# Kernel optimization log

Measured on AMD Instinct MI355X. Metric: run time of the kernel, lower is better.

Reference implementation:

```python
import jax, jax.numpy as jnp
import numpy as np

THRESH = 0.5   # global `thresh` used by ActFun
LENS = 0.5     # global `lens` (surrogate width)
DECAY = 0.25   # LIFNode init_decay
INV_STD = 1.0 / float(np.sqrt(1.0 + 1e-5))  # BN eval: running_mean=0, running_var=1
HEADS = 8
WINDOW = 8

@jax.custom_vjp
def act_fun(x):
    return (x > THRESH).astype(x.dtype)

def _act_fwd(x):
    return act_fun(x), x

def _act_bwd(x, g):
    temp = (jnp.abs(x - THRESH) < LENS).astype(g.dtype) / (2.0 * LENS)
    return (g * temp,)

act_fun.defvjp(_act_fwd, _act_bwd)

def lif(x):
    # x: [T, ...]; mem = x[0]; mem_t = mem_{t-1}*decay*(1-spike_{t-1}.detach()) + x_t
    spike0 = act_fun(x[0])
    def step(carry, xi):
        mem_prev, spike_prev = carry
        mem = mem_prev * DECAY * (1.0 - jax.lax.stop_gradient(spike_prev)) + xi
        spike = act_fun(mem)
        return (mem, spike), spike
    _, spikes = jax.lax.scan(step, (x[0], spike0), x[1:])
    return jnp.concatenate([spike0[None], spikes], axis=0)

def bn_eval(x, gamma, beta):
    # BatchNorm2d eval over channel D (last dim of [T,B,L,D]) with default running stats
    return x * (INV_STD * gamma) + beta

def linear(x, w, b):
    # torch nn.Linear: y = x @ w.T + b, w: [out, in]
    return jnp.einsum('tbld,ed->tble', x, w) + b


def setup_inputs() -> dict:
    key = jax.random.key(0)
    ks = jax.random.split(key, 12)
    T, B, L, D = 4, 4, 1024, 512
    s = 0.02
    inp = {
        'x': jax.random.normal(ks[0], (T, B, L, D), dtype=jnp.float32),
        'pos_bias': jax.random.uniform(ks[1], (L, L), dtype=jnp.float32),
        'q_w': jax.random.normal(ks[2], (D, D), dtype=jnp.float32) * s,
        'q_b': jnp.zeros((D,), jnp.float32),
        'q_g': jnp.ones((D,), jnp.float32),
        'q_beta': jnp.zeros((D,), jnp.float32),
        'k_w': jax.random.normal(ks[3], (D, D), dtype=jnp.float32) * s,
        'k_b': jnp.zeros((D,), jnp.float32),
        'k_g': jnp.ones((D,), jnp.float32),
        'k_beta': jnp.zeros((D,), jnp.float32),
        'v_w': jax.random.normal(ks[4], (D, D), dtype=jnp.float32) * s,
        'v_b': jnp.zeros((D,), jnp.float32),
        'v_g': jnp.ones((D,), jnp.float32),
        'v_beta': jnp.zeros((D,), jnp.float32),
        'last_w': jax.random.normal(ks[5], (D, D), dtype=jnp.float32) * s,
        'last_b': jnp.zeros((D,), jnp.float32),
        'last_g': jnp.ones((D,), jnp.float32),
        'last_beta': jnp.zeros((D,), jnp.float32),
    }
    return inp


def reference(x, pos_bias, q_w, q_b, q_g, q_beta, k_w, k_b, k_g, k_beta,
              v_w, v_b, v_g, v_beta, last_w, last_b, last_g, last_beta):
    T, B, L, D = x.shape
    H = HEADS
    Dh = D // H
    # local causal band: keep pos_bias[i,j] only where 0 <= i-j < WINDOW
    i = jnp.arange(L)[:, None]
    j = jnp.arange(L)[None, :]
    band = ((i - j) >= 0) & ((i - j) < WINDOW)
    pb = jnp.where(band, pos_bias[:L, :L], 0.0)  # [L, L]

    xs = lif(x)  # first_lif
    q = lif(bn_eval(linear(xs, q_w, q_b), q_g, q_beta))
    k = lif(bn_eval(linear(xs, k_w, k_b), k_g, k_beta))
    v = lif(bn_eval(linear(xs, v_w, v_b), v_g, v_beta))

    # [T,B,L,D] -> [T,B,L,H,Dh] -> [B,H,L,T,Dh] -> [B,H,L,T*Dh]
    qh = q.reshape(T, B, L, H, Dh).transpose(1, 3, 2, 0, 4).reshape(B, H, L, T * Dh)
    kv = (k * v).reshape(T, B, L, H, Dh).transpose(1, 3, 2, 0, 4).reshape(B, H, L, T * Dh)

    attn = jnp.einsum('ij,bhjd->bhid', pb, kv)  # local-window positional mixing
    out = qh * attn
    out = out.reshape(B, H, L, T, Dh).transpose(3, 0, 2, 1, 4).reshape(T, B, L, D)
    out = lif(out)  # attn_lif
    out = bn_eval(linear(out, last_w, last_b), last_g, last_beta)
    return out
```

## Files before the change

kernel.cpp:

```cpp
#include <hip/hip_runtime.h>
#include <stdint.h>


#define T_ 4
#define B_ 4
#define L_ 1024
#define D_ 512
#define BI_ (B_*L_)
#define STRIDE4 (B_*L_*D_/4)
#define INV_STD 0.9999950000374997f
#define EPS_FLAG 1e-3f
#define LIST_CAP 5000000u

typedef unsigned int   u32;
typedef unsigned char  u8;
typedef int i32x4 __attribute__((ext_vector_type(4)));

static __device__ __forceinline__ float spike_of(float m) {
  return m > 0.5f ? 1.0f : 0.0f;
}

__global__ __launch_bounds__(256) void k_wsplit(const float* __restrict__ qw,
    const float* __restrict__ kw, const float* __restrict__ vw,
    const float* __restrict__ lw, u8* __restrict__ Wq,
    float* __restrict__ scl, u32* __restrict__ cnt) {
  if (blockIdx.x == 0 && threadIdx.x == 0) *cnt = 0;
  int gid = blockIdx.x * 4 + (threadIdx.x >> 6);
  int mat = gid >> 9, e = gid & 511;
  int lane = threadIdx.x & 63;
  const float* W = mat == 0 ? qw : mat == 1 ? kw : mat == 2 ? vw : lw;
  const float4* w4 = (const float4*)(W + (size_t)e * 512 + lane * 8);
  float4 wa = w4[0], wb = w4[1];
  float w[8] = {wa.x, wa.y, wa.z, wa.w, wb.x, wb.y, wb.z, wb.w};
  float am = 0.f;
#pragma unroll
  for (int j = 0; j < 8; ++j) am = fmaxf(am, fabsf(w[j]));
#pragma unroll
  for (int off = 1; off < 64; off <<= 1)
    am = fmaxf(am, __shfl_xor(am, off, 64));
  float s1 = am > 0.f ? am * (1.0f / 127.0f) : 1.0f;
  float s2 = s1 * (1.0f / 254.0f);
  float inv1 = 1.0f / s1, inv2 = 1.0f / s2;
  u32 p1lo = 0, p1hi = 0, p2lo = 0, p2hi = 0;
#pragma unroll
  for (int j = 0; j < 8; ++j) {
    float q1 = rintf(w[j] * inv1);
    q1 = fminf(127.f, fmaxf(-127.f, q1));
    float r = w[j] - s1 * q1;
    float q2 = rintf(r * inv2);
    q2 = fminf(127.f, fmaxf(-127.f, q2));
    u32 b1 = (u32)(u8)(signed char)(int)q1;
    u32 b2 = (u32)(u8)(signed char)(int)q2;
    if (j < 4) { p1lo |= b1 << (j * 8); p2lo |= b2 << (j * 8); }
    else       { p1hi |= b1 << ((j - 4) * 8); p2hi |= b2 << ((j - 4) * 8); }
  }
  u8* base = Wq + (size_t)mat * 524288 + (size_t)(e >> 6) * 65536 +
             (size_t)(lane >> 1) * 1024 + (size_t)(e & 63) * 16 + (lane & 1) * 8;
  *(uint2*)base             = make_uint2(p1lo, p1hi);
  *(uint2*)(base + 32768)   = make_uint2(p2lo, p2hi);
  if (lane == 0) {
    scl[mat * 1024 + e] = s1;
    scl[mat * 1024 + 512 + e] = s2;
  }
}

__global__ __launch_bounds__(256) void k_lif_first(const float* __restrict__ x,
                                                   u8* __restrict__ xsb) {
  int idx = blockIdx.x * 256 + threadIdx.x;
  if (idx >= STRIDE4) return;
  const int bi = idx >> 7, d4 = idx & 127;
  const float4* x4 = (const float4*)x;
  uchar4* o4 = (uchar4*)xsb;
  float m[4], s[4];
  float4 v = x4[idx];
  m[0] = v.x; m[1] = v.y; m[2] = v.z; m[3] = v.w;
#pragma unroll
  for (int c = 0; c < 4; ++c) s[c] = spike_of(m[c]);
  o4[(bi * 4 + 0) * 128 + d4] =
      make_uchar4((u8)s[0], (u8)s[1], (u8)s[2], (u8)s[3]);
#pragma unroll
  for (int t = 1; t < T_; ++t) {
    v = x4[idx + t * STRIDE4];
    float xv[4] = {v.x, v.y, v.z, v.w};
#pragma unroll
    for (int c = 0; c < 4; ++c) {
      m[c] = m[c] * 0.25f * (1.0f - s[c]) + xv[c];
      s[c] = spike_of(m[c]);
    }
    o4[(bi * 4 + t) * 128 + d4] =
        make_uchar4((u8)s[0], (u8)s[1], (u8)s[2], (u8)s[3]);
  }
}

__device__ __forceinline__ void gemm_flat(const u8* __restrict__ Ab,
    const u8* __restrict__ Wc, int rowbase, int la, int lg,
    i32x4 (&acc)[4][4][2]) {
  const u8* ap = Ab + (size_t)(rowbase + la) * 512 + lg * 16;
  const u8* bp = Wc + lg * 1024 + la * 16;

#pragma unroll
  for (int s = 0; s < 4; ++s)
#pragma unroll
    for (int cf = 0; cf < 4; ++cf)
#pragma unroll
      for (int pl = 0; pl < 2; ++pl) acc[s][cf][pl] = (i32x4){0, 0, 0, 0};

  uint4 Abuf[2][4], Bbuf[2][8];
#pragma unroll
  for (int s = 0; s < 4; ++s)
    Abuf[0][s] = *(const uint4*)(ap + s * 8192);
#pragma unroll
  for (int cf = 0; cf < 4; ++cf)
#pragma unroll
    for (int pl = 0; pl < 2; ++pl)
      Bbuf[0][cf * 2 + pl] = *(const uint4*)(bp + pl * 32768 + cf * 256);

#pragma unroll
  for (int ks = 0; ks < 8; ++ks) {
    const int cur = ks & 1, nxt = cur ^ 1;
    if (ks < 7) {
#pragma unroll
      for (int s = 0; s < 4; ++s)
        Abuf[nxt][s] = *(const uint4*)(ap + s * 8192 + (ks + 1) * 64);
#pragma unroll
      for (int cf = 0; cf < 4; ++cf)
#pragma unroll
        for (int pl = 0; pl < 2; ++pl)
          Bbuf[nxt][cf * 2 + pl] =
              *(const uint4*)(bp + (ks + 1) * 4096 + pl * 32768 + cf * 256);
    }
#pragma unroll
    for (int cf = 0; cf < 4; ++cf)
#pragma unroll
      for (int pl = 0; pl < 2; ++pl)
#pragma unroll
        for (int s = 0; s < 4; ++s)
          acc[s][cf][pl] = __builtin_amdgcn_mfma_i32_16x16x64_i8(
              __builtin_bit_cast(i32x4, Abuf[cur][s]),
              __builtin_bit_cast(i32x4, Bbuf[cur][cf * 2 + pl]),
              acc[s][cf][pl], 0, 0, 0);
  }
}

__global__ __launch_bounds__(256) void k_gemm_qkv(const u8* __restrict__ Ab,
    const u8* __restrict__ Wq, const float* __restrict__ scl,
    const float* __restrict__ qb2, const float* __restrict__ qg,
    const float* __restrict__ qbe,
    const float* __restrict__ kb2, const float* __restrict__ kg,
    const float* __restrict__ kbe,
    const float* __restrict__ vb2, const float* __restrict__ vg,
    const float* __restrict__ vbe,
    u8* __restrict__ qs, u8* __restrict__ ks_, u8* __restrict__ vs,
    u32* __restrict__ list, u32* __restrict__ cnt) {
  const int tid = threadIdx.x;
  const int lane = tid & 63, wid = tid >> 6;
  const int la = lane & 15, lg = lane >> 4;
  const int colblk = blockIdx.x;
  const int tz = blockIdx.z;
  const int rowbase = (blockIdx.y * 4 + wid) * 64;
  const u8* Wc = Wq + (size_t)tz * 524288 + (size_t)colblk * 65536;
  const float* Bb = tz == 0 ? qb2 : tz == 1 ? kb2 : vb2;
  const float* Gg = tz == 0 ? qg  : tz == 1 ? kg  : vg;
  const float* Be = tz == 0 ? qbe : tz == 1 ? kbe : vbe;
  u8* S           = tz == 0 ? qs  : tz == 1 ? ks_ : vs;

  i32x4 acc[4][4][2];
  gemm_flat(Ab, Wc, rowbase, la, lg, acc);

#pragma unroll
  for (int cf = 0; cf < 4; ++cf) {
    int e = colblk * 64 + cf * 16 + la;
    float s1 = scl[tz * 1024 + e];
    float s2 = scl[tz * 1024 + 512 + e];
    float cs = INV_STD * Gg[e];
    float cb = Bb[e], ct = Be[e];
#pragma unroll
    for (int s = 0; s < 4; ++s) {
      int r0 = rowbase + s * 16 + lg * 4;
      int bi = r0 >> 2;
      float m = 0.f, sp = 0.f;
      int fl = 0;
#pragma unroll
      for (int p = 0; p < 4; ++p) {
        float raw = s1 * (float)acc[s][cf][0][p] + s2 * (float)acc[s][cf][1][p];
        float pre = (raw + cb) * cs + ct;
        if (p == 0) m = pre;
        else m = m * 0.25f * (1.0f - sp) + pre;
        sp = spike_of(m);
        if (fabsf(m - 0.5f) < EPS_FLAG) fl = 1;
        S[(size_t)(r0 + p) * 512 + e] = (u8)sp;
      }
      if (fl) {
        u32 pos = atomicAdd(cnt, 1u);
        if (pos < LIST_CAP)
          list[pos] = ((u32)tz << 21) | (u32)(bi * 512 + e);
      }
    }
  }
}

__global__ __launch_bounds__(256) void k_gemm_out(const u8* __restrict__ Ab,
    const u8* __restrict__ Wq, const float* __restrict__ scl,
    const float* __restrict__ bias, const float* __restrict__ gamma,
    const float* __restrict__ beta, float* __restrict__ Y) {
  const int tid = threadIdx.x;
  const int lane = tid & 63, wid = tid >> 6;
  const int la = lane & 15, lg = lane >> 4;
  const int colblk = blockIdx.x;
  const int rowbase = (blockIdx.y * 4 + wid) * 64;
  const u8* Wc = Wq + 3u * 524288 + (size_t)colblk * 65536;

  i32x4 acc[4][4][2];
  gemm_flat(Ab, Wc, rowbase, la, lg, acc);

#pragma unroll
  for (int cf = 0; cf < 4; ++cf) {
    int e = colblk * 64 + cf * 16 + la;
    float s1 = scl[3 * 1024 + e];
    float s2 = scl[3 * 1024 + 512 + e];
    float cs = INV_STD * gamma[e];
    float cb = bias[e], ct = beta[e];
#pragma unroll
    for (int s = 0; s < 4; ++s) {
      int r0 = rowbase + s * 16 + lg * 4;
      int bi = r0 >> 2;
#pragma unroll
      for (int p = 0; p < 4; ++p) {
        float raw = s1 * (float)acc[s][cf][0][p] + s2 * (float)acc[s][cf][1][p];
        Y[((size_t)p * BI_ + bi) * 512 + e] = (raw + cb) * cs + ct;
      }
    }
  }
}

__device__ __forceinline__ void consume32_u8(const float4 (&wb)[8],
                                             const uint4 (&ab)[2], float& c) {
#pragma unroll
  for (int u = 0; u < 8; ++u) {
    float4 w = wb[u];
    uint4 t = ab[u >> 2];
    u32 word = (u & 3) == 0 ? t.x : (u & 3) == 1 ? t.y
             : (u & 3) == 2 ? t.z : t.w;
    c += (word & 0xFFu)       ? w.x : 0.0f;
    c += (word & 0xFF00u)     ? w.y : 0.0f;
    c += (word & 0xFF0000u)   ? w.z : 0.0f;
    c += (word >> 24)         ? w.w : 0.0f;
  }
}

__global__ __launch_bounds__(128) void k_fixup_c(const u8* __restrict__ xsb,
    u8* __restrict__ qs, u8* __restrict__ ks, u8* __restrict__ vs,
    const float* __restrict__ qw, const float* __restrict__ qb2,
    const float* __restrict__ qg, const float* __restrict__ qbe,
    const float* __restrict__ kw, const float* __restrict__ kb2,
    const float* __restrict__ kg, const float* __restrict__ kbe,
    const float* __restrict__ vw, const float* __restrict__ vb2,
    const float* __restrict__ vg, const float* __restrict__ vbe,
    const u32* __restrict__ list, const u32* __restrict__ cnt) {
  u32 n = *cnt;
  if (n > LIST_CAP) n = LIST_CAP;
  u32 tot = n * 4;
  for (u32 ii = blockIdx.x * 128 + threadIdx.x; ii < tot;
       ii += gridDim.x * 128) {
    u32 i = ii >> 2;
    int t = (int)(ii & 3);
    u32 e = list[i];
    int tz = (int)(e >> 21);
    int col = (int)(e & 0x1FFFFFu);
    int bi = col >> 9, d = col & 511;
    const float* W  = tz == 0 ? qw  : tz == 1 ? kw  : vw;
    const float* Bb = tz == 0 ? qb2 : tz == 1 ? kb2 : vb2;
    const float* Gg = tz == 0 ? qg  : tz == 1 ? kg  : vg;
    const float* Be = tz == 0 ? qbe : tz == 1 ? kbe : vbe;
    u8* S           = tz == 0 ? qs  : tz == 1 ? ks  : vs;
    const float4* w4 = (const float4*)(W + (size_t)d * 512);
    const uint4*  R  = (const uint4*)(xsb + ((size_t)bi * 4 + t) * 512);

    float4 wA[8], wB[8];
    uint4 aA[2], aB[2];
#pragma unroll
    for (int u = 0; u < 8; ++u) wA[u] = w4[u];
#pragma unroll
    for (int u = 0; u < 2; ++u) aA[u] = R[u];
    float c = 0.f;
#pragma unroll
    for (int ch = 0; ch < 16; ++ch) {
      if ((ch & 1) == 0) {
        if (ch + 1 < 16) {
          int wb0 = (ch + 1) * 8, ab0 = (ch + 1) * 2;
#pragma unroll
          for (int u = 0; u < 8; ++u) wB[u] = w4[wb0 + u];
#pragma unroll
          for (int u = 0; u < 2; ++u) aB[u] = R[ab0 + u];
        }
        consume32_u8(wA, aA, c);
      } else {
        if (ch + 1 < 16) {
          int wb0 = (ch + 1) * 8, ab0 = (ch + 1) * 2;
#pragma unroll
          for (int u = 0; u < 8; ++u) wA[u] = w4[wb0 + u];
#pragma unroll
          for (int u = 0; u < 2; ++u) aA[u] = R[ab0 + u];
        }
        consume32_u8(wB, aB, c);
      }
    }
    int lane = threadIdx.x & 63;
    int qb = lane & ~3;
    float cq[4];
    cq[0] = __shfl(c, qb + 0, 64);
    cq[1] = __shfl(c, qb + 1, 64);
    cq[2] = __shfl(c, qb + 2, 64);
    cq[3] = __shfl(c, qb + 3, 64);
    float cs = INV_STD * Gg[d];
    float cb = Bb[d], ct = Be[d];
    float m = 0.f, s = 0.f;
    u8 myb = 0;
#pragma unroll
    for (int t2 = 0; t2 < 4; ++t2) {
      float pre = (cq[t2] + cb) * cs + ct;
      if (t2 == 0) m = pre;
      else m = m * 0.25f * (1.0f - s) + pre;
      s = spike_of(m);
      if (t2 == t) myb = (u8)s;
    }
    S[((size_t)bi * 4 + t) * 512 + d] = myb;
  }
}

__global__ __launch_bounds__(256) void k_attn(const u8* __restrict__ qs,
    const u8* __restrict__ ks, const u8* __restrict__ vs,
    const float* __restrict__ pos_bias, u8* __restrict__ sout) {
  int idx = blockIdx.x * 256 + threadIdx.x;
  if (idx >= STRIDE4) return;
  const int d4 = idx & 127;
  const int bi = idx >> 7;
  const int i = bi & (L_ - 1);
  const int wmax = i < 7 ? i : 7;

  float pbv[8];
  const float* pbrow = pos_bias + (size_t)i * L_ + i;
  for (int w = 0; w <= wmax; ++w) pbv[w] = pbrow[-w];

  const uchar4* k4 = (const uchar4*)ks;
  const uchar4* v4 = (const uchar4*)vs;
  const uchar4* q4 = (const uchar4*)qs;
  float pre[T_][4];

#pragma unroll
  for (int t = 0; t < T_; ++t) {
    float sum[4] = {0.f, 0.f, 0.f, 0.f};
    for (int w = wmax; w >= 0; --w) {
      int rj = ((bi - w) * 4 + t) * 128 + d4;
      uchar4 ku = k4[rj];
      uchar4 vu = v4[rj];
      sum[0] += (ku.x && vu.x) ? pbv[w] : 0.0f;
      sum[1] += (ku.y && vu.y) ? pbv[w] : 0.0f;
      sum[2] += (ku.z && vu.z) ? pbv[w] : 0.0f;
      sum[3] += (ku.w && vu.w) ? pbv[w] : 0.0f;
    }
    uchar4 qu = q4[(bi * 4 + t) * 128 + d4];
    pre[t][0] = qu.x ? sum[0] : 0.0f;
    pre[t][1] = qu.y ? sum[1] : 0.0f;
    pre[t][2] = qu.z ? sum[2] : 0.0f;
    pre[t][3] = qu.w ? sum[3] : 0.0f;
  }

  uchar4* s4 = (uchar4*)sout;
  float m[4], s[4];
#pragma unroll
  for (int c = 0; c < 4; ++c) { m[c] = pre[0][c]; s[c] = spike_of(m[c]); }
  s4[(bi * 4 + 0) * 128 + d4] =
      make_uchar4((u8)s[0], (u8)s[1], (u8)s[2], (u8)s[3]);
#pragma unroll
  for (int t = 1; t < T_; ++t) {
#pragma unroll
    for (int c = 0; c < 4; ++c) {
      m[c] = m[c] * 0.25f * (1.0f - s[c]) + pre[t][c];
      s[c] = spike_of(m[c]);
    }
    s4[(bi * 4 + t) * 128 + d4] =
        make_uchar4((u8)s[0], (u8)s[1], (u8)s[2], (u8)s[3]);
  }
}

extern "C" void kernel_launch(void* const* d_in, const int* in_sizes, int n_in,
                              void* d_out, int out_size, void* d_ws, size_t ws_size,
                              hipStream_t stream) {
  (void)in_sizes; (void)n_in; (void)out_size; (void)ws_size;
  const float* x        = (const float*)d_in[0];
  const float* pos_bias = (const float*)d_in[1];
  const float* q_w    = (const float*)d_in[2];
  const float* q_b    = (const float*)d_in[3];
  const float* q_g    = (const float*)d_in[4];
  const float* q_beta = (const float*)d_in[5];
  const float* k_w    = (const float*)d_in[6];
  const float* k_b    = (const float*)d_in[7];
  const float* k_g    = (const float*)d_in[8];
  const float* k_beta = (const float*)d_in[9];
  const float* v_w    = (const float*)d_in[10];
  const float* v_b    = (const float*)d_in[11];
  const float* v_g    = (const float*)d_in[12];
  const float* v_beta = (const float*)d_in[13];
  const float* last_w    = (const float*)d_in[14];
  const float* last_b    = (const float*)d_in[15];
  const float* last_g    = (const float*)d_in[16];
  const float* last_beta = (const float*)d_in[17];
  float* out = (float*)d_out;

  char* ws = (char*)d_ws;
  u8*    xsb  = (u8*)(ws + 0);
  u8*    qs   = (u8*)(ws + 8388608);
  u8*    ks   = (u8*)(ws + 16777216);
  u8*    vs   = (u8*)(ws + 25165824);
  u8*    sA   = (u8*)(ws + 33554432);
  u8*    Wq   = (u8*)(ws + 41943040);
  float* scl  = (float*)(ws + 46137344);
  u32*   list = (u32*)(ws + 50331648);
  u32*   cnt  = (u32*)(ws + 73400320);

  k_wsplit<<<512, 256, 0, stream>>>(q_w, k_w, v_w, last_w, Wq, scl, cnt);
  k_lif_first<<<2048, 256, 0, stream>>>(x, xsb);

  dim3 gq(8, 64, 3);
  k_gemm_qkv<<<gq, 256, 0, stream>>>(xsb, Wq, scl,
      q_b, q_g, q_beta, k_b, k_g, k_beta, v_b, v_g, v_beta,
      qs, ks, vs, list, cnt);

  k_fixup_c<<<2048, 128, 0, stream>>>(xsb, qs, ks, vs,
      q_w, q_b, q_g, q_beta, k_w, k_b, k_g, k_beta, v_w, v_b, v_g, v_beta,
      list, cnt);

  k_attn<<<2048, 256, 0, stream>>>(qs, ks, vs, pos_bias, sA);

  dim3 gg(8, 64);
  k_gemm_out<<<gg, 256, 0, stream>>>(sA, Wq, scl,
                                     last_b, last_g, last_beta, out);
}
```

Before: 346.2 us.

## Stage weight tile in LDS and coalesce spike stores via shared buffer

Both int8 GEMM kernels now copy their 64 KB weight column-block into LDS with global_load_lds before computing, and read B fragments from LDS instead of global memory. The A-operand double buffering is dropped in favour of direct per-step loads. The QKV kernel stages its spike outputs in a 16 KB shared tile and writes them back as coalesced 16-byte rows, and its grid order changes so blocks sharing a weight tile run close together. The cost is 80 KB of LDS per block, which limits occupancy, plus an up-front barrier-bound load phase.

```diff
diff --git a/kernel.cpp b/kernel.cpp
--- a/kernel.cpp
+++ b/kernel.cpp
@@ -18,6 +18,12 @@
 
 static __device__ __forceinline__ float spike_of(float m) {
   return m > 0.5f ? 1.0f : 0.0f;
+}
+
+__device__ __forceinline__ void gll16(const void* g, void* l) {
+  __builtin_amdgcn_global_load_lds(
+      (const __attribute__((address_space(1))) u32*)g,
+      (__attribute__((address_space(3))) u32*)l, 16, 0, 0);
 }
 
 __global__ __launch_bounds__(256) void k_wsplit(const float* __restrict__ qw,
@@ -92,43 +98,32 @@
   }
 }
 
-__device__ __forceinline__ void gemm_flat(const u8* __restrict__ Ab,
-    const u8* __restrict__ Wc, int rowbase, int la, int lg,
+__device__ __forceinline__ void gemm_wres(const u8* __restrict__ Ab,
+    const u8* __restrict__ smW, int rowbase, int la, int lg,
     i32x4 (&acc)[4][4][2]) {
+#pragma unroll
+  for (int s = 0; s < 4; ++s)
+#pragma unroll
+    for (int cf = 0; cf < 4; ++cf)
+#pragma unroll
+      for (int pl = 0; pl < 2; ++pl) acc[s][cf][pl] = (i32x4){0, 0, 0, 0};
+
   const u8* ap = Ab + (size_t)(rowbase + la) * 512 + lg * 16;
-  const u8* bp = Wc + lg * 1024 + la * 16;
-
-#pragma unroll
-  for (int s = 0; s < 4; ++s)
+  const u8* bp = smW + lg * 1024 + la * 16;
+
+#pragma unroll
+  for (int ks = 0; ks < 8; ++ks) {
+    uint4 Af[4];
+#pragma unroll
+    for (int s = 0; s < 4; ++s)
+      Af[s] = *(const uint4*)(ap + s * 8192 + ks * 64);
+    uint4 Bf[8];
 #pragma unroll
     for (int cf = 0; cf < 4; ++cf)
 #pragma unroll
-      for (int pl = 0; pl < 2; ++pl) acc[s][cf][pl] = (i32x4){0, 0, 0, 0};
-
-  uint4 Abuf[2][4], Bbuf[2][8];
-#pragma unroll
-  for (int s = 0; s < 4; ++s)
-    Abuf[0][s] = *(const uint4*)(ap + s * 8192);
-#pragma unroll
-  for (int cf = 0; cf < 4; ++cf)
-#pragma unroll
-    for (int pl = 0; pl < 2; ++pl)
-      Bbuf[0][cf * 2 + pl] = *(const uint4*)(bp + pl * 32768 + cf * 256);
-
-#pragma unroll
-  for (int ks = 0; ks < 8; ++ks) {
-    const int cur = ks & 1, nxt = cur ^ 1;
-    if (ks < 7) {
-#pragma unroll
-      for (int s = 0; s < 4; ++s)
-        Abuf[nxt][s] = *(const uint4*)(ap + s * 8192 + (ks + 1) * 64);
-#pragma unroll
-      for (int cf = 0; cf < 4; ++cf)
-#pragma unroll
-        for (int pl = 0; pl < 2; ++pl)
-          Bbuf[nxt][cf * 2 + pl] =
-              *(const uint4*)(bp + (ks + 1) * 4096 + pl * 32768 + cf * 256);
-    }
+      for (int pl = 0; pl < 2; ++pl)
+        Bf[cf * 2 + pl] =
+            *(const uint4*)(bp + pl * 32768 + ks * 4096 + cf * 256);
 #pragma unroll
     for (int cf = 0; cf < 4; ++cf)
 #pragma unroll
@@ -136,8 +131,8 @@
 #pragma unroll
         for (int s = 0; s < 4; ++s)
           acc[s][cf][pl] = __builtin_amdgcn_mfma_i32_16x16x64_i8(
-              __builtin_bit_cast(i32x4, Abuf[cur][s]),
-              __builtin_bit_cast(i32x4, Bbuf[cur][cf * 2 + pl]),
+              __builtin_bit_cast(i32x4, Af[s]),
+              __builtin_bit_cast(i32x4, Bf[cf * 2 + pl]),
               acc[s][cf][pl], 0, 0, 0);
   }
 }
@@ -152,20 +147,28 @@
     const float* __restrict__ vbe,
     u8* __restrict__ qs, u8* __restrict__ ks_, u8* __restrict__ vs,
     u32* __restrict__ list, u32* __restrict__ cnt) {
+  __shared__ __align__(16) u8 smW[65536];
+  __shared__ __align__(16) u8 smS[16384];
   const int tid = threadIdx.x;
   const int lane = tid & 63, wid = tid >> 6;
   const int la = lane & 15, lg = lane >> 4;
   const int colblk = blockIdx.x;
-  const int tz = blockIdx.z;
-  const int rowbase = (blockIdx.y * 4 + wid) * 64;
+  const int tz = blockIdx.y;
+  const int row0 = blockIdx.z * 256;
+  const int rowbase = row0 + wid * 64;
   const u8* Wc = Wq + (size_t)tz * 524288 + (size_t)colblk * 65536;
   const float* Bb = tz == 0 ? qb2 : tz == 1 ? kb2 : vb2;
   const float* Gg = tz == 0 ? qg  : tz == 1 ? kg  : vg;
   const float* Be = tz == 0 ? qbe : tz == 1 ? kbe : vbe;
   u8* S           = tz == 0 ? qs  : tz == 1 ? ks_ : vs;
 
+#pragma unroll
+  for (int u = 0; u < 16; ++u)
+    gll16(Wc + u * 4096 + tid * 16, smW + u * 4096 + tid * 16);
+  __syncthreads();
+
   i32x4 acc[4][4][2];
-  gemm_flat(Ab, Wc, rowbase, la, lg, acc);
+  gemm_wres(Ab, smW, rowbase, la, lg, acc);
 
 #pragma unroll
   for (int cf = 0; cf < 4; ++cf) {
@@ -176,8 +179,8 @@
     float cb = Bb[e], ct = Be[e];
 #pragma unroll
     for (int s = 0; s < 4; ++s) {
-      int r0 = rowbase + s * 16 + lg * 4;
-      int bi = r0 >> 2;
+      int rl = wid * 64 + s * 16 + lg * 4;
+      int bi = (row0 + rl) >> 2;
       float m = 0.f, sp = 0.f;
       int fl = 0;
 #pragma unroll
@@ -188,7 +191,7 @@
         else m = m * 0.25f * (1.0f - sp) + pre;
         sp = spike_of(m);
         if (fabsf(m - 0.5f) < EPS_FLAG) fl = 1;
-        S[(size_t)(r0 + p) * 512 + e] = (u8)sp;
+        smS[(rl + p) * 64 + cf * 16 + la] = (u8)sp;
       }
       if (fl) {
         u32 pos = atomicAdd(cnt, 1u);
@@ -197,21 +200,36 @@
       }
     }
   }
+  __syncthreads();
+#pragma unroll
+  for (int ps = 0; ps < 4; ++ps) {
+    int rr = ps * 64 + (tid >> 2);
+    int c16 = (tid & 3) * 16;
+    uint4 vv = *(const uint4*)(smS + rr * 64 + c16);
+    *(uint4*)(S + (size_t)(row0 + rr) * 512 + colblk * 64 + c16) = vv;
+  }
 }
 
 __global__ __launch_bounds__(256) void k_gemm_out(const u8* __restrict__ Ab,
     const u8* __restrict__ Wq, const float* __restrict__ scl,
     const float* __restrict__ bias, const float* __restrict__ gamma,
     const float* __restrict__ beta, float* __restrict__ Y) {
+  __shared__ __align__(16) u8 smW[65536];
   const int tid = threadIdx.x;
   const int lane = tid & 63, wid = tid >> 6;
   const int la = lane & 15, lg = lane >> 4;
   const int colblk = blockIdx.x;
-  const int rowbase = (blockIdx.y * 4 + wid) * 64;
+  const int row0 = blockIdx.y * 256;
+  const int rowbase = row0 + wid * 64;
   const u8* Wc = Wq + 3u * 524288 + (size_t)colblk * 65536;
 
+#pragma unroll
+  for (int u = 0; u < 16; ++u)
+    gll16(Wc + u * 4096 + tid * 16, smW + u * 4096 + tid * 16);
+  __syncthreads();
+
   i32x4 acc[4][4][2];
-  gemm_flat(Ab, Wc, rowbase, la, lg, acc);
+  gemm_wres(Ab, smW, rowbase, la, lg, acc);
 
 #pragma unroll
   for (int cf = 0; cf < 4; ++cf) {
@@ -422,7 +440,7 @@
   k_wsplit<<<512, 256, 0, stream>>>(q_w, k_w, v_w, last_w, Wq, scl, cnt);
   k_lif_first<<<2048, 256, 0, stream>>>(x, xsb);
 
-  dim3 gq(8, 64, 3);
+  dim3 gq(8, 3, 64);
   k_gemm_qkv<<<gq, 256, 0, stream>>>(xsb, Wq, scl,
       q_b, q_g, q_beta, k_b, k_g, k_beta, v_b, v_g, v_beta,
       qs, ks, vs, list, cnt);
```

New measurement: 323.9 us. -6.4%, faster.

## Stage spike rows in LDS and pack q/k/v spikes across time into u32

Applied to the files above, without the earlier changes.

The int8 GEMMs now load a 32-row activation tile into shared memory with global_load_lds and an XOR swizzle. Each block then computes all three q/k/v projections, or the full output width, for that tile. Weights are stored row-major and streamed per wave with register double buffering. The q/k/v spike outputs are packed with all four timesteps in one u32 per (position, channel), so attention loads each neighbour once for all timesteps and the GEMM epilogue does one 32-bit store. The cost is lower grid parallelism (512 blocks), heavier per-block work, and weight reads that are no longer staged in the tiled layout.

```diff
diff --git a/kernel.cpp b/kernel.cpp
--- a/kernel.cpp
+++ b/kernel.cpp
@@ -18,6 +18,12 @@
 
 static __device__ __forceinline__ float spike_of(float m) {
   return m > 0.5f ? 1.0f : 0.0f;
+}
+
+__device__ __forceinline__ void gll16(const void* g, void* l) {
+  __builtin_amdgcn_global_load_lds(
+      (const __attribute__((address_space(1))) u32*)g,
+      (__attribute__((address_space(3))) u32*)l, 16, 0, 0);
 }
 
 __global__ __launch_bounds__(256) void k_wsplit(const float* __restrict__ qw,
@@ -54,10 +60,9 @@
     if (j < 4) { p1lo |= b1 << (j * 8); p2lo |= b2 << (j * 8); }
     else       { p1hi |= b1 << ((j - 4) * 8); p2hi |= b2 << ((j - 4) * 8); }
   }
-  u8* base = Wq + (size_t)mat * 524288 + (size_t)(e >> 6) * 65536 +
-             (size_t)(lane >> 1) * 1024 + (size_t)(e & 63) * 16 + (lane & 1) * 8;
-  *(uint2*)base             = make_uint2(p1lo, p1hi);
-  *(uint2*)(base + 32768)   = make_uint2(p2lo, p2hi);
+  u8* base = Wq + (size_t)mat * 524288 + (size_t)e * 512 + lane * 8;
+  *(uint2*)base            = make_uint2(p1lo, p1hi);
+  *(uint2*)(base + 262144) = make_uint2(p2lo, p2hi);
   if (lane == 0) {
     scl[mat * 1024 + e] = s1;
     scl[mat * 1024 + 512 + e] = s2;
@@ -92,53 +97,40 @@
   }
 }
 
-__device__ __forceinline__ void gemm_flat(const u8* __restrict__ Ab,
-    const u8* __restrict__ Wc, int rowbase, int la, int lg,
-    i32x4 (&acc)[4][4][2]) {
-  const u8* ap = Ab + (size_t)(rowbase + la) * 512 + lg * 16;
-  const u8* bp = Wc + lg * 1024 + la * 16;
-
-#pragma unroll
-  for (int s = 0; s < 4; ++s)
-#pragma unroll
-    for (int cf = 0; cf < 4; ++cf)
-#pragma unroll
-      for (int pl = 0; pl < 2; ++pl) acc[s][cf][pl] = (i32x4){0, 0, 0, 0};
-
-  uint4 Abuf[2][4], Bbuf[2][8];
-#pragma unroll
-  for (int s = 0; s < 4; ++s)
-    Abuf[0][s] = *(const uint4*)(ap + s * 8192);
-#pragma unroll
-  for (int cf = 0; cf < 4; ++cf)
-#pragma unroll
-    for (int pl = 0; pl < 2; ++pl)
-      Bbuf[0][cf * 2 + pl] = *(const uint4*)(bp + pl * 32768 + cf * 256);
-
+__device__ __forceinline__ void loadw(uint4 (&buf)[8], const u8* wbase,
+                                      int pl, int ks) {
+#pragma unroll
+  for (int cf = 0; cf < 8; ++cf)
+    buf[cf] = *(const uint4*)(wbase + (size_t)pl * 262144 + cf * 8192 + ks * 64);
+}
+
+template <int PL>
+__device__ __forceinline__ void mm8(i32x4 (&acc)[8][2], uint4 aF,
+                                    const uint4 (&buf)[8]) {
+#pragma unroll
+  for (int cf = 0; cf < 8; ++cf)
+    acc[cf][PL] = __builtin_amdgcn_mfma_i32_16x16x64_i8(
+        __builtin_bit_cast(i32x4, aF), __builtin_bit_cast(i32x4, buf[cf]),
+        acc[cf][PL], 0, 0, 0);
+}
+
+__device__ __forceinline__ void pass_core(const u8* aRow, const u8* wbase,
+                                          int la, int lg, i32x4 (&acc)[8][2]) {
+#pragma unroll
+  for (int cf = 0; cf < 8; ++cf) {
+    acc[cf][0] = (i32x4){0, 0, 0, 0};
+    acc[cf][1] = (i32x4){0, 0, 0, 0};
+  }
+  uint4 b0[8], b1[8];
+  loadw(b0, wbase, 0, 0);
+  loadw(b1, wbase, 1, 0);
 #pragma unroll
   for (int ks = 0; ks < 8; ++ks) {
-    const int cur = ks & 1, nxt = cur ^ 1;
-    if (ks < 7) {
-#pragma unroll
-      for (int s = 0; s < 4; ++s)
-        Abuf[nxt][s] = *(const uint4*)(ap + s * 8192 + (ks + 1) * 64);
-#pragma unroll
-      for (int cf = 0; cf < 4; ++cf)
-#pragma unroll
-        for (int pl = 0; pl < 2; ++pl)
-          Bbuf[nxt][cf * 2 + pl] =
-              *(const uint4*)(bp + (ks + 1) * 4096 + pl * 32768 + cf * 256);
-    }
-#pragma unroll
-    for (int cf = 0; cf < 4; ++cf)
-#pragma unroll
-      for (int pl = 0; pl < 2; ++pl)
-#pragma unroll
-        for (int s = 0; s < 4; ++s)
-          acc[s][cf][pl] = __builtin_amdgcn_mfma_i32_16x16x64_i8(
-              __builtin_bit_cast(i32x4, Abuf[cur][s]),
-              __builtin_bit_cast(i32x4, Bbuf[cur][cf * 2 + pl]),
-              acc[s][cf][pl], 0, 0, 0);
+    uint4 aF = *(const uint4*)(aRow + ((((ks * 4 + lg) ^ (la & 7)) << 4)));
+    mm8<0>(acc, aF, b0);
+    if (ks < 7) loadw(b0, wbase, 0, ks + 1);
+    mm8<1>(acc, aF, b1);
+    if (ks < 7) loadw(b1, wbase, 1, ks + 1);
   }
 }
 
@@ -150,50 +142,66 @@
     const float* __restrict__ kbe,
     const float* __restrict__ vb2, const float* __restrict__ vg,
     const float* __restrict__ vbe,
-    u8* __restrict__ qs, u8* __restrict__ ks_, u8* __restrict__ vs,
+    u32* __restrict__ qs32, u32* __restrict__ ks32, u32* __restrict__ vs32,
     u32* __restrict__ list, u32* __restrict__ cnt) {
+  __shared__ __align__(16) u8 smA[16384];
   const int tid = threadIdx.x;
-  const int lane = tid & 63, wid = tid >> 6;
+  const int lane = tid & 63, w = tid >> 6;
   const int la = lane & 15, lg = lane >> 4;
-  const int colblk = blockIdx.x;
-  const int tz = blockIdx.z;
-  const int rowbase = (blockIdx.y * 4 + wid) * 64;
-  const u8* Wc = Wq + (size_t)tz * 524288 + (size_t)colblk * 65536;
-  const float* Bb = tz == 0 ? qb2 : tz == 1 ? kb2 : vb2;
-  const float* Gg = tz == 0 ? qg  : tz == 1 ? kg  : vg;
-  const float* Be = tz == 0 ? qbe : tz == 1 ? kbe : vbe;
-  u8* S           = tz == 0 ? qs  : tz == 1 ? ks_ : vs;
-
-  i32x4 acc[4][4][2];
-  gemm_flat(Ab, Wc, rowbase, la, lg, acc);
-
-#pragma unroll
-  for (int cf = 0; cf < 4; ++cf) {
-    int e = colblk * 64 + cf * 16 + la;
-    float s1 = scl[tz * 1024 + e];
-    float s2 = scl[tz * 1024 + 512 + e];
-    float cs = INV_STD * Gg[e];
-    float cb = Bb[e], ct = Be[e];
-#pragma unroll
-    for (int s = 0; s < 4; ++s) {
-      int r0 = rowbase + s * 16 + lg * 4;
-      int bi = r0 >> 2;
-      float m = 0.f, sp = 0.f;
-      int fl = 0;
-#pragma unroll
-      for (int p = 0; p < 4; ++p) {
-        float raw = s1 * (float)acc[s][cf][0][p] + s2 * (float)acc[s][cf][1][p];
-        float pre = (raw + cb) * cs + ct;
-        if (p == 0) m = pre;
-        else m = m * 0.25f * (1.0f - sp) + pre;
-        sp = spike_of(m);
-        if (fabsf(m - 0.5f) < EPS_FLAG) fl = 1;
-        S[(size_t)(r0 + p) * 512 + e] = (u8)sp;
-      }
-      if (fl) {
-        u32 pos = atomicAdd(cnt, 1u);
-        if (pos < LIST_CAP)
-          list[pos] = ((u32)tz << 21) | (u32)(bi * 512 + e);
+  const int row0 = blockIdx.x * 32;
+
+#pragma unroll
+  for (int u = 0; u < 4; ++u) {
+    int lin = u * 4096 + tid * 16;
+    int r = lin >> 9, slot = (lin >> 4) & 31;
+    gll16(Ab + (size_t)(row0 + r) * 512 + ((slot ^ (r & 7)) << 4), smA + lin);
+  }
+  __syncthreads();
+
+  const int rsub = (w & 1) * 16;
+  const int colh = (w >> 1) * 256;
+  const u8* aRow = smA + (size_t)(rsub + la) * 512;
+  const int bi = (row0 >> 2) + (w & 1) * 4 + lg;
+
+  for (int mat = 0; mat < 3; ++mat) {
+    const float* Bb = mat == 0 ? qb2 : mat == 1 ? kb2 : vb2;
+    const float* Gg = mat == 0 ? qg  : mat == 1 ? kg  : vg;
+    const float* Be = mat == 0 ? qbe : mat == 1 ? kbe : vbe;
+    u32* S32        = mat == 0 ? qs32 : mat == 1 ? ks32 : vs32;
+#pragma unroll
+    for (int cb = 0; cb < 2; ++cb) {
+      const int colbase = colh + cb * 128;
+      const u8* wbase = Wq + (size_t)mat * 524288 +
+                        (size_t)(colbase + la) * 512 + lg * 16;
+      i32x4 acc[8][2];
+      pass_core(aRow, wbase, la, lg, acc);
+
+#pragma unroll
+      for (int cf = 0; cf < 8; ++cf) {
+        int e = colbase + cf * 16 + la;
+        float s1 = scl[mat * 1024 + e];
+        float s2 = scl[mat * 1024 + 512 + e];
+        float csx = INV_STD * Gg[e];
+        float cbx = Bb[e], ctx = Be[e];
+        float m = 0.f, sp = 0.f;
+        u32 pk = 0;
+        int fl = 0;
+#pragma unroll
+        for (int p = 0; p < 4; ++p) {
+          float raw = s1 * (float)acc[cf][0][p] + s2 * (float)acc[cf][1][p];
+          float pre = (raw + cbx) * csx + ctx;
+          if (p == 0) m = pre;
+          else m = m * 0.25f * (1.0f - sp) + pre;
+          sp = spike_of(m);
+          if (fabsf(m - 0.5f) < EPS_FLAG) fl = 1;
+          pk |= (u32)(sp != 0.0f) << (p * 8);
+        }
+        S32[(size_t)bi * 512 + e] = pk;
+        if (fl) {
+          u32 pos = atomicAdd(cnt, 1u);
+          if (pos < LIST_CAP)
+            list[pos] = ((u32)mat << 21) | (u32)(bi * 512 + e);
+        }
       }
     }
   }
@@ -203,31 +211,43 @@
     const u8* __restrict__ Wq, const float* __restrict__ scl,
     const float* __restrict__ bias, const float* __restrict__ gamma,
     const float* __restrict__ beta, float* __restrict__ Y) {
+  __shared__ __align__(16) u8 smA[16384];
   const int tid = threadIdx.x;
-  const int lane = tid & 63, wid = tid >> 6;
+  const int lane = tid & 63, w = tid >> 6;
   const int la = lane & 15, lg = lane >> 4;
-  const int colblk = blockIdx.x;
-  const int rowbase = (blockIdx.y * 4 + wid) * 64;
-  const u8* Wc = Wq + 3u * 524288 + (size_t)colblk * 65536;
-
-  i32x4 acc[4][4][2];
-  gemm_flat(Ab, Wc, rowbase, la, lg, acc);
-
-#pragma unroll
-  for (int cf = 0; cf < 4; ++cf) {
-    int e = colblk * 64 + cf * 16 + la;
-    float s1 = scl[3 * 1024 + e];
-    float s2 = scl[3 * 1024 + 512 + e];
-    float cs = INV_STD * gamma[e];
-    float cb = bias[e], ct = beta[e];
-#pragma unroll
-    for (int s = 0; s < 4; ++s) {
-      int r0 = rowbase + s * 16 + lg * 4;
-      int bi = r0 >> 2;
+  const int row0 = blockIdx.x * 32;
+
+#pragma unroll
+  for (int u = 0; u < 4; ++u) {
+    int lin = u * 4096 + tid * 16;
+    int r = lin >> 9, slot = (lin >> 4) & 31;
+    gll16(Ab + (size_t)(row0 + r) * 512 + ((slot ^ (r & 7)) << 4), smA + lin);
+  }
+  __syncthreads();
+
+  const int rsub = (w & 1) * 16;
+  const int colh = (w >> 1) * 256;
+  const u8* aRow = smA + (size_t)(rsub + la) * 512;
+  const int bi = (row0 >> 2) + (w & 1) * 4 + lg;
+
+#pragma unroll
+  for (int cb = 0; cb < 2; ++cb) {
+    const int colbase = colh + cb * 128;
+    const u8* wbase = Wq + 3u * 524288 + (size_t)(colbase + la) * 512 + lg * 16;
+    i32x4 acc[8][2];
+    pass_core(aRow, wbase, la, lg, acc);
+
+#pragma unroll
+    for (int cf = 0; cf < 8; ++cf) {
+      int e = colbase + cf * 16 + la;
+      float s1 = scl[3 * 1024 + e];
+      float s2 = scl[3 * 1024 + 512 + e];
+      float csx = INV_STD * gamma[e];
+      float cbx = bias[e], ctx = beta[e];
 #pragma unroll
       for (int p = 0; p < 4; ++p) {
-        float raw = s1 * (float)acc[s][cf][0][p] + s2 * (float)acc[s][cf][1][p];
-        Y[((size_t)p * BI_ + bi) * 512 + e] = (raw + cb) * cs + ct;
+        float raw = s1 * (float)acc[cf][0][p] + s2 * (float)acc[cf][1][p];
+        Y[((size_t)p * BI_ + bi) * 512 + e] = (raw + cbx) * csx + ctx;
       }
     }
   }
@@ -249,7 +269,7 @@
 }
 
 __global__ __launch_bounds__(128) void k_fixup_c(const u8* __restrict__ xsb,
-    u8* __restrict__ qs, u8* __restrict__ ks, u8* __restrict__ vs,
+    u32* __restrict__ qs32, u32* __restrict__ ks32, u32* __restrict__ vs32,
     const float* __restrict__ qw, const float* __restrict__ qb2,
     const float* __restrict__ qg, const float* __restrict__ qbe,
     const float* __restrict__ kw, const float* __restrict__ kb2,
@@ -272,7 +292,7 @@
     const float* Bb = tz == 0 ? qb2 : tz == 1 ? kb2 : vb2;
     const float* Gg = tz == 0 ? qg  : tz == 1 ? kg  : vg;
     const float* Be = tz == 0 ? qbe : tz == 1 ? kbe : vbe;
-    u8* S           = tz == 0 ? qs  : tz == 1 ? ks  : vs;
+    u32* S          = tz == 0 ? qs32 : tz == 1 ? ks32 : vs32;
     const float4* w4 = (const float4*)(W + (size_t)d * 512);
     const uint4*  R  = (const uint4*)(xsb + ((size_t)bi * 4 + t) * 512);
 
@@ -324,12 +344,12 @@
       s = spike_of(m);
       if (t2 == t) myb = (u8)s;
     }
-    S[((size_t)bi * 4 + t) * 512 + d] = myb;
-  }
-}
-
-__global__ __launch_bounds__(256) void k_attn(const u8* __restrict__ qs,
-    const u8* __restrict__ ks, const u8* __restrict__ vs,
+    ((u8*)S)[((size_t)bi * 512 + d) * 4 + t] = myb;
+  }
+}
+
+__global__ __launch_bounds__(256) void k_attn(const u32* __restrict__ qs32,
+    const u32* __restrict__ ks32, const u32* __restrict__ vs32,
     const float* __restrict__ pos_bias, u8* __restrict__ sout) {
   int idx = blockIdx.x * 256 + threadIdx.x;
   if (idx >= STRIDE4) return;
@@ -342,29 +362,37 @@
   const float* pbrow = pos_bias + (size_t)i * L_ + i;
   for (int w = 0; w <= wmax; ++w) pbv[w] = pbrow[-w];
 
-  const uchar4* k4 = (const uchar4*)ks;
-  const uchar4* v4 = (const uchar4*)vs;
-  const uchar4* q4 = (const uchar4*)qs;
-  float pre[T_][4];
-
-#pragma unroll
-  for (int t = 0; t < T_; ++t) {
-    float sum[4] = {0.f, 0.f, 0.f, 0.f};
-    for (int w = wmax; w >= 0; --w) {
-      int rj = ((bi - w) * 4 + t) * 128 + d4;
-      uchar4 ku = k4[rj];
-      uchar4 vu = v4[rj];
-      sum[0] += (ku.x && vu.x) ? pbv[w] : 0.0f;
-      sum[1] += (ku.y && vu.y) ? pbv[w] : 0.0f;
-      sum[2] += (ku.z && vu.z) ? pbv[w] : 0.0f;
-      sum[3] += (ku.w && vu.w) ? pbv[w] : 0.0f;
-    }
-    uchar4 qu = q4[(bi * 4 + t) * 128 + d4];
-    pre[t][0] = qu.x ? sum[0] : 0.0f;
-    pre[t][1] = qu.y ? sum[1] : 0.0f;
-    pre[t][2] = qu.z ? sum[2] : 0.0f;
-    pre[t][3] = qu.w ? sum[3] : 0.0f;
-  }
+  const uint4* k4 = (const uint4*)ks32;
+  const uint4* v4 = (const uint4*)vs32;
+  const uint4* q4 = (const uint4*)qs32;
+
+  float sum[4][4];
+#pragma unroll
+  for (int t = 0; t < 4; ++t)
+#pragma unroll
+    for (int c = 0; c < 4; ++c) sum[t][c] = 0.f;
+
+  for (int w = wmax; w >= 0; --w) {
+    uint4 ku = k4[(size_t)(bi - w) * 128 + d4];
+    uint4 vu = v4[(size_t)(bi - w) * 128 + d4];
+    float pb = pbv[w];
+    u32 kw[4] = {ku.x, ku.y, ku.z, ku.w};
+    u32 vw[4] = {vu.x, vu.y, vu.z, vu.w};
+#pragma unroll
+    for (int c = 0; c < 4; ++c)
+#pragma unroll
+      for (int t = 0; t < 4; ++t)
+        if (((kw[c] >> (t * 8)) & 255u) && ((vw[c] >> (t * 8)) & 255u))
+          sum[t][c] += pb;
+  }
+  uint4 qu = q4[(size_t)bi * 128 + d4];
+  u32 qw[4] = {qu.x, qu.y, qu.z, qu.w};
+  float pre[4][4];
+#pragma unroll
+  for (int t = 0; t < 4; ++t)
+#pragma unroll
+    for (int c = 0; c < 4; ++c)
+      pre[t][c] = ((qw[c] >> (t * 8)) & 255u) ? sum[t][c] : 0.f;
 
   uchar4* s4 = (uchar4*)sout;
   float m[4], s[4];
@@ -410,9 +438,9 @@
 
   char* ws = (char*)d_ws;
   u8*    xsb  = (u8*)(ws + 0);
-  u8*    qs   = (u8*)(ws + 8388608);
-  u8*    ks   = (u8*)(ws + 16777216);
-  u8*    vs   = (u8*)(ws + 25165824);
+  u32*   qs32 = (u32*)(ws + 8388608);
+  u32*   ks32 = (u32*)(ws + 16777216);
+  u32*   vs32 = (u32*)(ws + 25165824);
   u8*    sA   = (u8*)(ws + 33554432);
   u8*    Wq   = (u8*)(ws + 41943040);
   float* scl  = (float*)(ws + 46137344);
@@ -422,18 +450,16 @@
   k_wsplit<<<512, 256, 0, stream>>>(q_w, k_w, v_w, last_w, Wq, scl, cnt);
   k_lif_first<<<2048, 256, 0, stream>>>(x, xsb);
 
-  dim3 gq(8, 64, 3);
-  k_gemm_qkv<<<gq, 256, 0, stream>>>(xsb, Wq, scl,
+  k_gemm_qkv<<<512, 256, 0, stream>>>(xsb, Wq, scl,
       q_b, q_g, q_beta, k_b, k_g, k_beta, v_b, v_g, v_beta,
-      qs, ks, vs, list, cnt);
-
-  k_fixup_c<<<2048, 128, 0, stream>>>(xsb, qs, ks, vs,
+      qs32, ks32, vs32, list, cnt);
+
+  k_fixup_c<<<2048, 128, 0, stream>>>(xsb, qs32, ks32, vs32,
       q_w, q_b, q_g, q_beta, k_w, k_b, k_g, k_beta, v_w, v_b, v_g, v_beta,
       list, cnt);
 
-  k_attn<<<2048, 256, 0, stream>>>(qs, ks, vs, pos_bias, sA);
-
-  dim3 gg(8, 64);
-  k_gemm_out<<<gg, 256, 0, stream>>>(sA, Wq, scl,
-                                     last_b, last_g, last_beta, out);
-}
+  k_attn<<<2048, 256, 0, stream>>>(qs32, ks32, vs32, pos_bias, sA);
+
+  k_gemm_out<<<512, 256, 0, stream>>>(sA, Wq, scl,
+                                      last_b, last_g, last_beta, out);
+}
```

Result: slower. 432.8 us (+25.0%).
